# Kernel optimization log

Measured on AMD Instinct MI355X. Metric: run time of the kernel, lower is better.

Reference implementation:

```python
import jax, jax.numpy as jnp
import numpy as np

# ---- dims (match init_kwargs) ----
B0, C0, H0, W0 = 16, 64, 128, 128
G = 8            # d_model of inner Mamba2
D_STATE = 16
D_CONV = 3
EXPAND = 2
HEADDIM = 8
D_INNER = EXPAND * G            # 16
NHEADS = D_INNER // HEADDIM     # 2
NGROUPS = 1
CONV_DIM = D_INNER + 2 * NGROUPS * D_STATE   # 48
D_IN_PROJ = 2 * D_INNER + 2 * NGROUPS * D_STATE + NHEADS  # 66
EPS = 1e-5


def silu(x):
    return x * jax.nn.sigmoid(x)


def setup_inputs() -> dict:
    key = jax.random.key(0)
    ks = jax.random.split(key, 12)
    s = 0.02
    return {
        "x": jax.random.normal(ks[0], (B0, C0, H0, W0), jnp.float32),
        # 1x1 conv tokenize / detokenize (stored as matrices)
        "w_tok": jax.random.normal(ks[1], (G, C0), jnp.float32) * s,
        "b_tok": jnp.zeros((G,), jnp.float32),
        "w_detok": jax.random.normal(ks[2], (C0, G), jnp.float32) * s,
        "b_detok": jnp.zeros((C0,), jnp.float32),
        # Mamba2 params
        "w_in": jax.random.normal(ks[3], (D_IN_PROJ, G), jnp.float32) * s,
        "w_conv": jax.random.normal(ks[4], (CONV_DIM, 1, D_CONV), jnp.float32) * s,
        "b_conv": jnp.zeros((CONV_DIM,), jnp.float32),
        "dt_bias": jax.random.uniform(ks[5], (NHEADS,), jnp.float32, -4.0, -2.0),
        "A_log": jnp.log(jnp.arange(1, NHEADS + 1, dtype=jnp.float32)),
        "D": jnp.ones((NHEADS,), jnp.float32),
        "norm_w": jnp.ones((D_INNER,), jnp.float32),
        "w_out": jax.random.normal(ks[6], (G, D_INNER), jnp.float32) * s,
    }


def _mamba2(u, w_in, w_conv, b_conv, dt_bias, A_log, D, norm_w, w_out):
    # u: [B, L, G]
    Bb, L, _ = u.shape
    zxbcdt = jnp.einsum('blg,dg->bld', u, w_in)                 # [B,L,66]
    z = zxbcdt[..., :D_INNER]                                   # [B,L,16]
    xBC = zxbcdt[..., D_INNER:D_INNER + CONV_DIM]               # [B,L,48]
    dt = jax.nn.softplus(zxbcdt[..., D_INNER + CONV_DIM:] + dt_bias)  # [B,L,H]

    # causal depthwise conv1d over time
    xBC_t = jnp.moveaxis(xBC, 1, 2)                             # [B,48,L]
    xBC_t = jnp.pad(xBC_t, ((0, 0), (0, 0), (D_CONV - 1, 0)))
    xBC_t = jax.lax.conv_general_dilated(
        xBC_t, w_conv, window_strides=(1,), padding='VALID',
        dimension_numbers=('NCH', 'OIH', 'NCH'), feature_group_count=CONV_DIM)
    xBC = silu(jnp.moveaxis(xBC_t + b_conv[None, :, None], 1, 2))  # [B,L,48]

    xh = xBC[..., :D_INNER].reshape(Bb, L, NHEADS, HEADDIM)     # [B,L,H,P]
    Bm = xBC[..., D_INNER:D_INNER + D_STATE]                    # [B,L,N] (ngroups=1)
    Cm = xBC[..., D_INNER + D_STATE:]                           # [B,L,N]

    A = -jnp.exp(A_log)                                         # [H]
    dA = jnp.exp(dt * A)                                        # [B,L,H]

    # time-major sequential selective scan
    def step(state, inp):
        dA_t, dt_t, x_t, B_t, C_t = inp  # [B,H],[B,H],[B,H,P],[B,N],[B,N]
        state = state * dA_t[:, :, None, None] \
            + (dt_t[:, :, None] * x_t)[..., None] * B_t[:, None, None, :]
        y = jnp.einsum('bhpn,bn->bhp', state, C_t)
        return state, y

    init = jnp.zeros((Bb, NHEADS, HEADDIM, D_STATE), u.dtype)
    xs = (jnp.moveaxis(dA, 1, 0), jnp.moveaxis(dt, 1, 0),
          jnp.moveaxis(xh, 1, 0), jnp.moveaxis(Bm, 1, 0), jnp.moveaxis(Cm, 1, 0))
    _, ys = jax.lax.scan(step, init, xs)                        # [L,B,H,P]
    y = jnp.moveaxis(ys, 0, 1) + D[None, None, :, None] * xh    # [B,L,H,P]
    y = y.reshape(Bb, L, D_INNER)

    # gated RMSNorm then out projection
    y = y * silu(z)
    y = y * jax.lax.rsqrt(jnp.mean(y * y, axis=-1, keepdims=True) + EPS) * norm_w
    return jnp.einsum('bld,gd->blg', y, w_out)


def reference(x, w_tok, b_tok, w_detok, b_detok, w_in, w_conv, b_conv,
              dt_bias, A_log, D, norm_w, w_out):
    Bb, C, H, W = x.shape
    g = jnp.einsum('bchw,gc->bghw', x, w_tok) + b_tok[None, :, None, None]
    g = g.reshape(Bb, G, H * W).transpose(0, 2, 1)              # [B,HW,G]
    g = _mamba2(g, w_in, w_conv, b_conv, dt_bias, A_log, D, norm_w, w_out) + g
    g = g.transpose(0, 2, 1).reshape(Bb, G, H, W)
    return x + jnp.einsum('bghw,cg->bchw', g, w_detok) + b_detok[None, :, None, None]
```

## Files before the change

kernel.cpp:

```cpp
#include <hip/hip_runtime.h>

namespace {
constexpr int NB   = 16;
constexpr int NC   = 64;
constexpr int HW   = 128*128;
constexpr int SL   = 16384;
constexpr int CQ   = 64;
constexpr int NCH  = SL/CQ;
constexpr int PWV  = 9728;

typedef short short8 __attribute__((ext_vector_type(8)));
typedef float f32x4  __attribute__((ext_vector_type(4)));

__device__ __forceinline__ float frcp(float x){ return __builtin_amdgcn_rcpf(x); }
__device__ __forceinline__ float rl(float v, int s){
  return __int_as_float(__builtin_amdgcn_readlane(__float_as_int(v), s));
}
__device__ __forceinline__ float sigu(float a){ return frcp(1.0f + __expf(-a)); }
__device__ __forceinline__ float softplusf(float a){
  return fmaxf(a, 0.f) + __logf(1.f + __expf(-fabsf(a)));
}
__device__ __forceinline__ unsigned bfr(float x){
  unsigned u = __float_as_uint(x);
  u = u + 0x7FFF + ((u>>16)&1);
  return u>>16;
}
__device__ __forceinline__ unsigned pk2(float a, float b){
  return (bfr(a)&0xFFFFu) | (bfr(b)<<16);
}
__device__ __forceinline__ float blo(unsigned u){ return __uint_as_float(u<<16); }
__device__ __forceinline__ float bhi(unsigned u){ return __uint_as_float(u & 0xFFFF0000u); }
union CV8 { unsigned u[4]; short8 s; };

__global__ __launch_bounds__(256) void k_tok(
    const float* __restrict__ x, const float* __restrict__ w_tok,
    const float* __restrict__ b_tok, float* __restrict__ g0,
    const float* __restrict__ w_in, const float* __restrict__ w_conv,
    unsigned short* __restrict__ weff)
{
  if (blockIdx.x == 0) {
    for (int i = threadIdx.x; i < 64*32; i += 256) {
      int j = i >> 5, k = i & 31;
      float v = 0.f;
      if (j < 48) {
        if (k < 24) v = w_conv[j*3 + (k>>3)] * w_in[(16+j)*8 + (k&7)];
      } else if (j < 50) {
        if (k >= 16 && k < 24) v = w_in[(64 + (j-48))*8 + (k-16)];
      }
      weff[i] = (unsigned short)bfr(v);
    }
  }
  __shared__ float s_wt[NC][8];
  __shared__ float s_bt[8];
  for (int i = threadIdx.x; i < NC*8; i += 256) s_wt[i>>3][i&7] = w_tok[(i&7)*NC + (i>>3)];
  if (threadIdx.x < 8) s_bt[threadIdx.x] = b_tok[threadIdx.x];
  __syncthreads();
  long idx = (long)blockIdx.x * 256 + threadIdx.x;
  int b = (int)(idx >> 14);
  int l = (int)(idx & (SL-1));
  float acc[8];
  #pragma unroll
  for (int g = 0; g < 8; ++g) acc[g] = s_bt[g];
  const float* xp = x + (long)b*NC*HW + l;
  #pragma unroll 8
  for (int c = 0; c < NC; ++c) {
    float v = xp[(long)c*HW];
    const float4* wr = (const float4*)s_wt[c];
    float4 w0 = wr[0], w1 = wr[1];
    acc[0] += v*w0.x; acc[1] += v*w0.y; acc[2] += v*w0.z; acc[3] += v*w0.w;
    acc[4] += v*w1.x; acc[5] += v*w1.y; acc[6] += v*w1.z; acc[7] += v*w1.w;
  }
  float* gp = g0 + idx*8;
  *(float4*)gp     = make_float4(acc[0],acc[1],acc[2],acc[3]);
  *(float4*)(gp+4) = make_float4(acc[4],acc[5],acc[6],acc[7]);
}

__global__ __launch_bounds__(256) void k_front(
    const float* __restrict__ g0, const unsigned short* __restrict__ weff,
    const float* __restrict__ b_conv,
    const float* __restrict__ dt_bias, const float* __restrict__ A_log,
    const float* __restrict__ Dvec,
    float* __restrict__ Sc, float* __restrict__ Pc,
    float* __restrict__ ceg, unsigned short* __restrict__ Cg,
    float* __restrict__ Yg)
{
  __shared__ float s_bc[48];
  __shared__ float s_misc[8];
  __shared__ char  s_wv[4][PWV];

  int tid = threadIdx.x, lane = tid & 63, wave = tid >> 6;
  int c15 = lane & 15, lg = lane >> 4;

  if (tid < 48) s_bc[tid] = b_conv[tid];
  if (tid < 2) {
    s_misc[tid]   = -__expf(A_log[tid]);
    s_misc[2+tid] = dt_bias[tid];
    s_misc[4+tid] = Dvec[tid];
  }
  __syncthreads();

  int b   = blockIdx.x >> 6;
  int chB = (blockIdx.x & 63)*4 + wave;
  long cg = (long)b*NCH + chB;
  int l0  = chB*CQ;
  char* WR = s_wv[wave];
  char* BT  = WR;
  char* uB  = WR + 2048;
  char* uC  = WR + 4096;
  char* Xp  = WR + 6144;
  char* Mb  = WR;
  char* ytr = WR;
  char* dtL = WR + 8192;
  char* cfL = WR + 8704;
  char* ceL = WR + 9216;

  short8 zero8 = {0,0,0,0,0,0,0,0};
  f32x4  zero4 = {0.f,0.f,0.f,0.f};

  short8 Af[4];
  #pragma unroll
  for (int tt = 0; tt < 4; ++tt) {
    int p = l0 + 16*tt + c15 - 2 + lg;
    bool ok = (lg < 3) && (p >= 0);
    const float* up = g0 + ((long)b*SL + (ok ? p : 0))*8;
    float4 a = *(const float4*)up, c = *(const float4*)(up+4);
    CV8 w;
    w.u[0] = pk2(a.x,a.y); w.u[1] = pk2(a.z,a.w);
    w.u[2] = pk2(c.x,c.y); w.u[3] = pk2(c.z,c.w);
    Af[tt] = ok ? w.s : zero8;
  }

  f32x4 xg[4];
  #pragma unroll
  for (int jj = 0; jj < 4; ++jj) {
    short8 Wf = *(const short8*)(weff + (16*jj + c15)*32 + lg*8);
    f32x4 o[4];
    #pragma unroll
    for (int tt = 0; tt < 4; ++tt)
      o[tt] = __builtin_amdgcn_mfma_f32_16x16x32_bf16(Af[tt], Wf, zero4, 0,0,0);
    if (jj == 3) {
      if (c15 < 2) {
        float bias = s_misc[2+c15];
        #pragma unroll
        for (int tt = 0; tt < 4; ++tt) {
          #pragma unroll
          for (int r = 0; r < 4; ++r)
            *(float*)(dtL + c15*256 + (16*tt + 4*lg + r)*4) = o[tt][r] + bias;
        }
      }
    } else {
      float bias = s_bc[16*jj + c15];
      #pragma unroll
      for (int tt = 0; tt < 4; ++tt) {
        float s0 = (o[tt][0]+bias), s1 = (o[tt][1]+bias);
        float s2 = (o[tt][2]+bias), s3 = (o[tt][3]+bias);
        s0 *= sigu(s0); s1 *= sigu(s1); s2 *= sigu(s2); s3 *= sigu(s3);
        int t0 = 16*tt + 4*lg;
        if (jj == 0) {
          f32x4 v; v[0]=s0; v[1]=s1; v[2]=s2; v[3]=s3;
          xg[tt] = v;
        } else if (jj == 1) {
          uint2 wv; wv.x = pk2(s0,s1); wv.y = pk2(s2,s3);
          *(uint2*)(BT + c15*128 + ((t0*2) ^ ((c15&7)<<4))) = wv;
          *(short*)(uB + (t0  )*32 + c15*2) = (short)bfr(s0);
          *(short*)(uB + (t0+1)*32 + c15*2) = (short)bfr(s1);
          *(short*)(uB + (t0+2)*32 + c15*2) = (short)bfr(s2);
          *(short*)(uB + (t0+3)*32 + c15*2) = (short)bfr(s3);
        } else {
          *(short*)(uC + (t0  )*32 + c15*2) = (short)bfr(s0);
          *(short*)(uC + (t0+1)*32 + c15*2) = (short)bfr(s1);
          *(short*)(uC + (t0+2)*32 + c15*2) = (short)bfr(s2);
          *(short*)(uC + (t0+3)*32 + c15*2) = (short)bfr(s3);
        }
      }
    }
  }
  __builtin_amdgcn_wave_barrier();
  __builtin_amdgcn_sched_barrier(0x7F);

  float dt0 = softplusf(*(const float*)(dtL + lane*4));
  float dt1 = softplusf(*(const float*)(dtL + 256 + lane*4));
  float c0 = s_misc[0]*dt0, c1 = s_misc[1]*dt1;
  #pragma unroll
  for (int off = 1; off < 64; off <<= 1) {
    float t0 = __shfl_up(c0, off), t1 = __shfl_up(c1, off);
    if (lane >= off) { c0 += t0; c1 += t1; }
  }
  float ce0 = __expf(c0), ce1 = __expf(c1);
  float cf0 = __expf(-c0)*dt0, cf1 = __expf(-c1)*dt1;
  float cee0 = rl(ce0, 63), cee1 = rl(ce1, 63);
  ceg[cg*128 + lane]      = ce0;
  ceg[cg*128 + 64 + lane] = ce1;
  if (lane == 0) { Pc[cg*2] = cee0; Pc[cg*2+1] = cee1; }
  *(float*)(cfL + lane*4)       = cf0;
  *(float*)(cfL + 256 + lane*4) = cf1;
  *(float*)(ceL + lane*4)       = ce0;
  *(float*)(ceL + 256 + lane*4) = ce1;
  __builtin_amdgcn_wave_barrier();
  __builtin_amdgcn_sched_barrier(0x7F);

  int hh = (c15 < 8) ? 0 : 1;
  #pragma unroll
  for (int tt = 0; tt < 4; ++tt) {
    int t0 = 16*tt + 4*lg;
    float4 cf4 = *(const float4*)(cfL + hh*256 + t0*4);
    uint2 wv;
    wv.x = pk2(cf4.x*xg[tt][0], cf4.y*xg[tt][1]);
    wv.y = pk2(cf4.z*xg[tt][2], cf4.w*xg[tt][3]);
    *(uint2*)(Xp + c15*128 + ((t0*2) ^ ((c15&7)<<4))) = wv;
  }
  __builtin_amdgcn_wave_barrier();
  __builtin_amdgcn_sched_barrier(0x7F);

  { short8 ca = *(const short8*)(uC + lane*32);
    short8 cb = *(const short8*)(uC + lane*32 + 16);
    *(short8*)(Cg + cg*1024 + lane*16)     = ca;
    *(short8*)(Cg + cg*1024 + lane*16 + 8) = cb; }

  { f32x4 sacc = zero4;
    #pragma unroll
    for (int kb = 0; kb < 2; ++kb) {
      int cb2 = (64*kb + 16*lg) ^ ((c15&7)<<4);
      short8 Afx = *(const short8*)(Xp + c15*128 + cb2);
      short8 Bfx = *(const short8*)(BT + c15*128 + cb2);
      sacc = __builtin_amdgcn_mfma_f32_16x16x32_bf16(Afx, Bfx, sacc, 0,0,0);
    }
    float cee = (lg < 2) ? cee0 : cee1;
    #pragma unroll
    for (int r = 0; r < 4; ++r)
      Sc[cg*256 + (4*lg+r)*16 + c15] = cee*sacc[r];
  }

  short8 Cfr[4], Bfr[4], Xf[2];
  #pragma unroll
  for (int tt = 0; tt < 4; ++tt) {
    Cfr[tt] = zero8; Bfr[tt] = zero8;
    if (lg < 2) {
      Cfr[tt] = *(const short8*)(uC + (16*tt + c15)*32 + 16*lg);
      Bfr[tt] = *(const short8*)(uB + (16*tt + c15)*32 + 16*lg);
    }
  }
  #pragma unroll
  for (int kb = 0; kb < 2; ++kb)
    Xf[kb] = *(const short8*)(Xp + c15*128 + ((64*kb + 16*lg) ^ ((c15&7)<<4)));
  __builtin_amdgcn_wave_barrier();
  __builtin_amdgcn_sched_barrier(0x7F);

  #pragma unroll
  for (int tt = 0; tt < 4; ++tt) {
    int t  = 16*tt + c15;
    int sw = (t&7)<<4;
    #pragma unroll
    for (int ts = 0; ts < 4; ++ts) {
      if (ts <= tt) {
        f32x4 gA = __builtin_amdgcn_mfma_f32_16x16x32_bf16(Bfr[ts], Cfr[tt], zero4, 0,0,0);
        if (ts == tt) {
          #pragma unroll
          for (int r = 0; r < 4; ++r)
            gA[r] = (4*lg + r <= c15) ? gA[r] : 0.f;
        }
        uint2 wv; wv.x = pk2(gA[0],gA[1]); wv.y = pk2(gA[2],gA[3]);
        *(uint2*)(Mb + t*128 + ((32*ts + 8*lg) ^ sw)) = wv;
      }
    }
    if (tt == 0 || tt == 2) {
      uint2 zv; zv.x = 0u; zv.y = 0u;
      *(uint2*)(Mb + t*128 + ((32*(tt+1) + 8*lg) ^ sw)) = zv;
    }
  }
  __builtin_amdgcn_wave_barrier();
  __builtin_amdgcn_sched_barrier(0x7F);

  f32x4 acc[4];
  #pragma unroll
  for (int tt = 0; tt < 4; ++tt) acc[tt] = zero4;
  #pragma unroll
  for (int tt = 0; tt < 4; ++tt) {
    int t = 16*tt + c15, sw = (t&7)<<4;
    { short8 Mf = *(const short8*)(Mb + t*128 + ((16*lg) ^ sw));
      acc[tt] = __builtin_amdgcn_mfma_f32_16x16x32_bf16(Mf, Xf[0], acc[tt], 0,0,0); }
    if (tt >= 2) {
      short8 Mf = *(const short8*)(Mb + t*128 + ((64 + 16*lg) ^ sw));
      acc[tt] = __builtin_amdgcn_mfma_f32_16x16x32_bf16(Mf, Xf[1], acc[tt], 0,0,0);
    }
  }
  __builtin_amdgcn_sched_barrier(0x7F);

  float Dh = (c15 < 8) ? s_misc[4] : s_misc[5];
  #pragma unroll
  for (int tt = 0; tt < 4; ++tt) {
    int t0 = 16*tt + 4*lg;
    float4 ce4 = *(const float4*)(ceL + hh*256 + t0*4);
    *(float*)(ytr + (t0  )*96 + c15*4) = ce4.x*acc[tt][0] + Dh*xg[tt][0];
    *(float*)(ytr + (t0+1)*96 + c15*4) = ce4.y*acc[tt][1] + Dh*xg[tt][1];
    *(float*)(ytr + (t0+2)*96 + c15*4) = ce4.z*acc[tt][2] + Dh*xg[tt][2];
    *(float*)(ytr + (t0+3)*96 + c15*4) = ce4.w*acc[tt][3] + Dh*xg[tt][3];
  }
  __builtin_amdgcn_wave_barrier();
  __builtin_amdgcn_sched_barrier(0x7F);

  float* yg = Yg + cg*1024 + lane*16;
  #pragma unroll
  for (int i = 0; i < 4; ++i) {
    float4 q = *(const float4*)(ytr + lane*96 + i*16);
    *(float4*)(yg + 4*i) = q;
  }
}

__global__ __launch_bounds__(256) void k_scan(
    const float* __restrict__ Sc, const float* __restrict__ Pc,
    float* __restrict__ Stin)
{
  int b = blockIdx.x;
  int tid = threadIdx.x;
  int h = tid >> 7;
  float st = 0.f;
  long base = (long)b * NCH;
  #pragma unroll 8
  for (int c = 0; c < NCH; ++c) {
    Stin[(base + c)*256 + tid] = st;
    st = st * Pc[(base + c)*2 + h] + Sc[(base + c)*256 + tid];
  }
}

__global__ __launch_bounds__(256) void k_out(
    const float* __restrict__ g0, const float* __restrict__ w_in,
    const float* __restrict__ norm_w, const float* __restrict__ w_out,
    const float* __restrict__ Stin, const float* __restrict__ ceg,
    const unsigned short* __restrict__ Cg, const float* __restrict__ Yg,
    const float* __restrict__ x, const float* __restrict__ w_detok,
    const float* __restrict__ b_detok, float* __restrict__ out)
{
  __shared__ float s_win[16][8];
  __shared__ float s_wout[8][16];
  __shared__ float s_nw[16];
  __shared__ float s_wd[NC][8];
  __shared__ float s_bd[NC];
  __shared__ float s_st[4][256];

  int tid = threadIdx.x, lane = tid & 63, wave = tid >> 6;
  if (tid < 128) s_win[tid>>3][tid&7] = w_in[tid];
  if (tid < 128) s_wout[tid>>4][tid&15] = w_out[tid];
  if (tid < 16)  s_nw[tid] = norm_w[tid];
  for (int i = tid; i < NC*8; i += 256) s_wd[i>>3][i&7] = w_detok[i];
  if (tid < NC) s_bd[tid] = b_detok[tid];
  __syncthreads();

  auto dot8 = [&](const float* uu, int row) -> float {
    const float4* wr = (const float4*)s_win[row];
    float4 w0 = wr[0], w1 = wr[1];
    return uu[0]*w0.x + uu[1]*w0.y + uu[2]*w0.z + uu[3]*w0.w
         + uu[4]*w1.x + uu[5]*w1.y + uu[6]*w1.z + uu[7]*w1.w;
  };

  int b   = blockIdx.x >> 6;
  int chB = (blockIdx.x & 63)*4 + wave;
  long cg = (long)b*NCH + chB;
  int l   = chB*CQ + lane;
  long pos = (long)b*SL + l;

  { float4 t4 = *(const float4*)(Stin + cg*256 + lane*4);
    *(float4*)&s_st[wave][lane*4] = t4; }

  float u[8];
  { const float* up = g0 + pos*8;
    float4 a = *(const float4*)up, c = *(const float4*)(up+4);
    u[0]=a.x;u[1]=a.y;u[2]=a.z;u[3]=a.w;u[4]=c.x;u[5]=c.y;u[6]=c.z;u[7]=c.w; }

  float Cr[16];
  { const uint4* cp = (const uint4*)(Cg + cg*1024 + lane*16);
    uint4 ca = cp[0], cb = cp[1];
    Cr[0]=blo(ca.x); Cr[1]=bhi(ca.x); Cr[2]=blo(ca.y); Cr[3]=bhi(ca.y);
    Cr[4]=blo(ca.z); Cr[5]=bhi(ca.z); Cr[6]=blo(ca.w); Cr[7]=bhi(ca.w);
    Cr[8]=blo(cb.x); Cr[9]=bhi(cb.x); Cr[10]=blo(cb.y); Cr[11]=bhi(cb.y);
    Cr[12]=blo(cb.z); Cr[13]=bhi(cb.z); Cr[14]=blo(cb.w); Cr[15]=bhi(cb.w); }

  float yr[16];
  { const float* yp = Yg + cg*1024 + lane*16;
    #pragma unroll
    for (int i = 0; i < 4; ++i) {
      float4 q = *(const float4*)(yp + 4*i);
      yr[4*i]=q.x; yr[4*i+1]=q.y; yr[4*i+2]=q.z; yr[4*i+3]=q.w;
    } }
  float ce0t = ceg[cg*128 + lane];
  float ce1t = ceg[cg*128 + 64 + lane];

  __builtin_amdgcn_wave_barrier();
  __builtin_amdgcn_sched_barrier(0x7F);

  const float* st = &s_st[wave][0];
  float y[16];
  #pragma unroll
  for (int hp = 0; hp < 16; ++hp) {
    const float4* sp = (const float4*)(st + hp*16);
    float4 s0 = sp[0], s1 = sp[1], s2 = sp[2], s3 = sp[3];
    float a = Cr[0]*s0.x + Cr[1]*s0.y + Cr[2]*s0.z + Cr[3]*s0.w
            + Cr[4]*s1.x + Cr[5]*s1.y + Cr[6]*s1.z + Cr[7]*s1.w
            + Cr[8]*s2.x + Cr[9]*s2.y + Cr[10]*s2.z + Cr[11]*s2.w
            + Cr[12]*s3.x + Cr[13]*s3.y + Cr[14]*s3.z + Cr[15]*s3.w;
    y[hp] = yr[hp] + ((hp < 8) ? ce0t : ce1t)*a;
  }

  float yv[16]; float ss = 0.f;
  #pragma unroll
  for (int d = 0; d < 16; ++d) {
    float zz = dot8(u, d);
    float v = y[d] * (zz * sigu(zz));
    yv[d] = v; ss += v*v;
  }
  float scn = rsqrtf(ss*(1.f/16.f) + 1e-5f);
  { const float4* nw = (const float4*)s_nw;
    float4 n0 = nw[0], n1 = nw[1], n2 = nw[2], n3 = nw[3];
    yv[0]*=scn*n0.x; yv[1]*=scn*n0.y; yv[2]*=scn*n0.z; yv[3]*=scn*n0.w;
    yv[4]*=scn*n1.x; yv[5]*=scn*n1.y; yv[6]*=scn*n1.z; yv[7]*=scn*n1.w;
    yv[8]*=scn*n2.x; yv[9]*=scn*n2.y; yv[10]*=scn*n2.z; yv[11]*=scn*n2.w;
    yv[12]*=scn*n3.x; yv[13]*=scn*n3.y; yv[14]*=scn*n3.z; yv[15]*=scn*n3.w; }
  float og[8];
  #pragma unroll
  for (int g = 0; g < 8; ++g) {
    const float4* wr = (const float4*)s_wout[g];
    float4 w0 = wr[0], w1 = wr[1], w2 = wr[2], w3 = wr[3];
    float a = u[g];
    a += yv[0]*w0.x + yv[1]*w0.y + yv[2]*w0.z + yv[3]*w0.w;
    a += yv[4]*w1.x + yv[5]*w1.y + yv[6]*w1.z + yv[7]*w1.w;
    a += yv[8]*w2.x + yv[9]*w2.y + yv[10]*w2.z + yv[11]*w2.w;
    a += yv[12]*w3.x + yv[13]*w3.y + yv[14]*w3.z + yv[15]*w3.w;
    og[g] = a;
  }

  const float* xp = x + (long)b*NC*HW + l;
  float* op = out + (long)b*NC*HW + l;
  #pragma unroll 4
  for (int c = 0; c < NC; ++c) {
    const float4* wr = (const float4*)s_wd[c];
    float4 w0 = wr[0], w1 = wr[1];
    float a = s_bd[c] + xp[(long)c*HW];
    a += og[0]*w0.x + og[1]*w0.y + og[2]*w0.z + og[3]*w0.w;
    a += og[4]*w1.x + og[5]*w1.y + og[6]*w1.z + og[7]*w1.w;
    op[(long)c*HW] = a;
  }
}
}

extern "C" void kernel_launch(void* const* d_in, const int* in_sizes, int n_in,
                              void* d_out, int out_size, void* d_ws, size_t ws_size,
                              hipStream_t stream)
{
  const float* x       = (const float*)d_in[0];
  const float* w_tok   = (const float*)d_in[1];
  const float* b_tok   = (const float*)d_in[2];
  const float* w_detok = (const float*)d_in[3];
  const float* b_detok = (const float*)d_in[4];
  const float* w_in    = (const float*)d_in[5];
  const float* w_conv  = (const float*)d_in[6];
  const float* b_conv  = (const float*)d_in[7];
  const float* dt_bias = (const float*)d_in[8];
  const float* A_log   = (const float*)d_in[9];
  const float* Dvec    = (const float*)d_in[10];
  const float* norm_w  = (const float*)d_in[11];
  const float* w_out   = (const float*)d_in[12];
  float* out = (float*)d_out;

  float* ws   = (float*)d_ws;
  float* g0   = ws;
  float* Sc   = g0 + (long)NB*SL*8;
  float* Pc   = Sc + (long)NB*NCH*256;
  float* Stin = Pc + (long)NB*NCH*2;
  float* ceg  = Stin + (long)NB*NCH*256;
  float* Yg   = ceg + (long)NB*NCH*128;
  unsigned short* Cg = (unsigned short*)(Yg + (long)NB*NCH*1024);
  unsigned short* weff = Cg + (long)NB*NCH*1024;

  k_tok<<<NB*SL/256, 256, 0, stream>>>(x, w_tok, b_tok, g0, w_in, w_conv, weff);
  k_front<<<NB*NCH/4, 256, 0, stream>>>(g0, weff, b_conv, dt_bias,
                                        A_log, Dvec, Sc, Pc, ceg, Cg, Yg);
  k_scan<<<NB, 256, 0, stream>>>(Sc, Pc, Stin);
  k_out<<<NB*NCH/4, 256, 0, stream>>>(g0, w_in, norm_w, w_out,
                                      Stin, ceg, Cg, Yg,
                                      x, w_detok, b_detok, out);
}
```

Measured before the change: 94.18 us.

## Stage detokenize inputs in shared memory and vectorize x/out accesses per channel

The output stage now writes each position's 8 gated outputs to shared memory, synchronizes, and remaps threads so each group of four threads handles one channel over the block's 256 positions. Each thread issues float4 loads and stores of x and out instead of scalar per-channel strided accesses, and keeps the detok weights in registers. This targets the memory-bound read of x and write of out, which dominate traffic, at the cost of an extra block barrier and 8KB of shared memory.

```diff
diff --git a/kernel.cpp b/kernel.cpp
--- a/kernel.cpp
+++ b/kernel.cpp
@@ -334,16 +334,13 @@
   __shared__ float s_win[16][8];
   __shared__ float s_wout[8][16];
   __shared__ float s_nw[16];
-  __shared__ float s_wd[NC][8];
-  __shared__ float s_bd[NC];
   __shared__ float s_st[4][256];
+  __shared__ float s_og[8][256];
 
   int tid = threadIdx.x, lane = tid & 63, wave = tid >> 6;
   if (tid < 128) s_win[tid>>3][tid&7] = w_in[tid];
   if (tid < 128) s_wout[tid>>4][tid&15] = w_out[tid];
   if (tid < 16)  s_nw[tid] = norm_w[tid];
-  for (int i = tid; i < NC*8; i += 256) s_wd[i>>3][i&7] = w_detok[i];
-  if (tid < NC) s_bd[tid] = b_detok[tid];
   __syncthreads();
 
   auto dot8 = [&](const float* uu, int row) -> float {
@@ -356,8 +353,7 @@
   int b   = blockIdx.x >> 6;
   int chB = (blockIdx.x & 63)*4 + wave;
   long cg = (long)b*NCH + chB;
-  int l   = chB*CQ + lane;
-  long pos = (long)b*SL + l;
+  long pos = (long)b*SL + chB*CQ + lane;
 
   { float4 t4 = *(const float4*)(Stin + cg*256 + lane*4);
     *(float4*)&s_st[wave][lane*4] = t4; }
@@ -415,7 +411,7 @@
     yv[4]*=scn*n1.x; yv[5]*=scn*n1.y; yv[6]*=scn*n1.z; yv[7]*=scn*n1.w;
     yv[8]*=scn*n2.x; yv[9]*=scn*n2.y; yv[10]*=scn*n2.z; yv[11]*=scn*n2.w;
     yv[12]*=scn*n3.x; yv[13]*=scn*n3.y; yv[14]*=scn*n3.z; yv[15]*=scn*n3.w; }
-  float og[8];
+  int posL = wave*64 + lane;
   #pragma unroll
   for (int g = 0; g < 8; ++g) {
     const float4* wr = (const float4*)s_wout[g];
@@ -425,19 +421,34 @@
     a += yv[4]*w1.x + yv[5]*w1.y + yv[6]*w1.z + yv[7]*w1.w;
     a += yv[8]*w2.x + yv[9]*w2.y + yv[10]*w2.z + yv[11]*w2.w;
     a += yv[12]*w3.x + yv[13]*w3.y + yv[14]*w3.z + yv[15]*w3.w;
-    og[g] = a;
-  }
-
-  const float* xp = x + (long)b*NC*HW + l;
-  float* op = out + (long)b*NC*HW + l;
+    s_og[g][posL] = a;
+  }
+  __syncthreads();
+
+  int c  = tid >> 2;
+  int qq = tid & 3;
+  int l0b = (blockIdx.x & 63) * 256;
+  const float* xp = x + (long)b*NC*HW + (long)c*HW + l0b;
+  float* op = out + (long)b*NC*HW + (long)c*HW + l0b;
+  float wd[8];
+  { float4 wa = *(const float4*)(w_detok + c*8);
+    float4 wb = *(const float4*)(w_detok + c*8 + 4);
+    wd[0]=wa.x; wd[1]=wa.y; wd[2]=wa.z; wd[3]=wa.w;
+    wd[4]=wb.x; wd[5]=wb.y; wd[6]=wb.z; wd[7]=wb.w; }
+  float bd = b_detok[c];
+
   #pragma unroll 4
-  for (int c = 0; c < NC; ++c) {
-    const float4* wr = (const float4*)s_wd[c];
-    float4 w0 = wr[0], w1 = wr[1];
-    float a = s_bd[c] + xp[(long)c*HW];
-    a += og[0]*w0.x + og[1]*w0.y + og[2]*w0.z + og[3]*w0.w;
-    a += og[4]*w1.x + og[5]*w1.y + og[6]*w1.z + og[7]*w1.w;
-    op[(long)c*HW] = a;
+  for (int k = 0; k < 16; ++k) {
+    int q = qq + 4*k;
+    float4 xv = *(const float4*)(xp + q*4);
+    float r0 = xv.x + bd, r1 = xv.y + bd, r2 = xv.z + bd, r3 = xv.w + bd;
+    #pragma unroll
+    for (int g = 0; g < 8; ++g) {
+      float4 o4 = *(const float4*)&s_og[g][q*4];
+      r0 += o4.x*wd[g]; r1 += o4.y*wd[g];
+      r2 += o4.z*wd[g]; r3 += o4.w*wd[g];
+    }
+    *(float4*)(op + q*4) = make_float4(r0,r1,r2,r3);
   }
 }
 }
```

New measurement: 99.93 us. 1.06x slower.
